# Kernel optimization log

Measured on AMD Instinct MI355X. Metric: run time of the kernel, lower is better.

The kernel has to match this reference:

```python
import jax, jax.numpy as jnp
import numpy as np

N, D, K = 32768, 256, 2048
BETA = 0.25  # init arg beta, in [0,1) branch of the loss


def setup_inputs() -> dict:
    key = jax.random.key(0)
    k1, k2 = jax.random.split(key)
    x = jax.random.normal(k1, (N, D), dtype=jnp.float32)
    # mimics nn.Embedding init: uniform(-1/K, 1/K) then mean-centered
    cb = jax.random.uniform(k2, (K, D), dtype=jnp.float32, minval=-1.0 / K, maxval=1.0 / K)
    codebook = cb - cb.mean(axis=0)
    return {"x": x, "codebook": codebook}


def reference(x, codebook):
    # pairwise squared L2 distances: [N, K]
    dist = (
        jnp.sum(x * x, axis=1, keepdims=True)
        + jnp.sum(codebook * codebook, axis=1)
        - 2.0 * jnp.matmul(x, codebook.T)
    )
    encoding_inds = jnp.argmin(dist, axis=1)  # [N]
    # one-hot @ codebook == gather of nearest code vectors
    x_codebook = jnp.take(codebook, encoding_inds, axis=0)  # [N, D]
    # straight-through quantization
    x_quantized = x + jax.lax.stop_gradient(x_codebook - x)
    # VQ loss, beta in [0, 1) branch
    commit = jnp.mean((x - jax.lax.stop_gradient(x_codebook)) ** 2)
    embed = jnp.mean((x_codebook - jax.lax.stop_gradient(x)) ** 2)
    loss = BETA * commit + embed
    return x_quantized, loss
```

## Files before the change

### kernel.cpp

```cpp
#include <hip/hip_runtime.h>

#define N_ROWS 32768
#define DIM    256
#define KCODES 2048
#define CSCALE 4096.0f

typedef __attribute__((ext_vector_type(16))) float f32x16;
typedef __attribute__((ext_vector_type(4)))  unsigned int u32x4;

union frag16 { u32x4 v; long l[2]; };

#define WAIT_LGKM0 0xC07F
#define WAIT_VM4   0x0F74
#define WAIT_VM0   0x0F70

__device__ __forceinline__ void gl16(const void* g, void* l) {
    __builtin_amdgcn_global_load_lds(
        (const __attribute__((address_space(1))) unsigned int*)g,
        (__attribute__((address_space(3))) unsigned int*)l, 16, 0, 0);
}

__device__ __forceinline__ uint4 pack16(const float* s) {
    int a = __builtin_amdgcn_cvt_pk_fp8_f32(s[0],  s[1],  0, false);
    a     = __builtin_amdgcn_cvt_pk_fp8_f32(s[2],  s[3],  a, true);
    int b = __builtin_amdgcn_cvt_pk_fp8_f32(s[4],  s[5],  0, false);
    b     = __builtin_amdgcn_cvt_pk_fp8_f32(s[6],  s[7],  b, true);
    int c = __builtin_amdgcn_cvt_pk_fp8_f32(s[8],  s[9],  0, false);
    c     = __builtin_amdgcn_cvt_pk_fp8_f32(s[10], s[11], c, true);
    int d = __builtin_amdgcn_cvt_pk_fp8_f32(s[12], s[13], 0, false);
    d     = __builtin_amdgcn_cvt_pk_fp8_f32(s[14], s[15], d, true);
    uint4 o; o.x = a; o.y = b; o.z = c; o.w = d;
    return o;
}


__global__ void prep_cb(const float* __restrict__ cb, unsigned int* __restrict__ cbf8,
                        float* __restrict__ halfcn, float* __restrict__ loss) {
    const int t    = threadIdx.x;
    const int code = blockIdx.x * 4 + (t >> 6);
    const int s    = t & 63;
    if (blockIdx.x == 0 && t == 0) *loss = 0.0f;
    const int kc = s >> 4, d = (s >> 2) & 3, b4 = (s & 3) * 4;
    const int h = d >> 1, q = d & 1;
    const int k0 = kc * 64 + q * 32 + (b4 >> 3) * 16 + h * 8 + (b4 & 7);
    float4 v = *(const float4*)&cb[(size_t)code * DIM + k0];
    int pk = __builtin_amdgcn_cvt_pk_fp8_f32(v.x * CSCALE, v.y * CSCALE, 0, false);
    pk     = __builtin_amdgcn_cvt_pk_fp8_f32(v.z * CSCALE, v.w * CSCALE, pk, true);
    cbf8[(size_t)code * 64 + s] = (unsigned int)pk;
    float ssum = v.x * v.x + v.y * v.y + v.z * v.z + v.w * v.w;
    #pragma unroll
    for (int o = 32; o > 0; o >>= 1) ssum += __shfl_down(ssum, o, 64);
    if (s == 0) halfcn[code] = 0.5f * CSCALE * ssum;
}

__global__ __launch_bounds__(256, 2) void vq_fused(
        const float* __restrict__ x, const float* __restrict__ cb,
        const char* __restrict__ cbf8, const float* __restrict__ halfcn,
        float* __restrict__ out, float* __restrict__ loss) {
    __shared__ char As[4][4096];
    __shared__ char Bs[2][4][4096];
    __shared__ float red[64][4];
    __shared__ int  idxs[64];
    __shared__ float lred[4];

    const int t    = threadIdx.x;
    const int lane = t & 63;
    const int w    = t >> 6;
    const int l32  = lane & 31;
    const int h    = lane >> 5;
    const int row0 = blockIdx.x * 64;

    {
        const int r   = t >> 2;
        const int kc  = t & 3;
        const int key = (r >> 1) & 3;
        const float* src = x + (size_t)(row0 + r) * DIM + kc * 64;
        float buf[16];
        #pragma unroll
        for (int p = 0; p < 4; p++) {
            const int d = p ^ key, hh = d >> 1, qq = d & 1;
            #pragma unroll
            for (int j = 0; j < 4; j++) *(float4*)(buf + j * 4) =
                *(const float4*)(src + qq * 32 + (j >> 1) * 16 + hh * 8 + (j & 1) * 4);
            *(uint4*)(As[kc] + r * 64 + p * 16) = pack16(buf);
        }
    }

    float hcv[8][2];
    #pragma unroll
    for (int p = 0; p < 8; p++) {
        hcv[p][0] = halfcn[p * 256 + w * 64 + l32];
        hcv[p][1] = halfcn[p * 256 + w * 64 + 32 + l32];
    }

    const int lsub = lane >> 2;
    const int lpos = lane & 3;
    auto stageB = [&](int i) {
        const int pass = i >> 2, kc = i & 3;
        char* dst = Bs[i & 1][w];
        #pragma unroll
        for (int r_ = 0; r_ < 4; r_++) {
            const int lc = r_ * 16 + lsub;
            const int g  = lpos ^ ((lc >> 1) & 3);
            const char* src = cbf8 + (size_t)(pass * 256 + w * 64 + lc) * 256
                              + kc * 64 + g * 16;
            gl16(src, dst + r_ * 1024);
        }
    };

    float mp[2][16];
    #pragma unroll
    for (int rt = 0; rt < 2; rt++)
        #pragma unroll
        for (int r = 0; r < 16; r++) mp[rt][r] = -3.0e38f;

    const int key = (l32 >> 1) & 3;
    const int p0  = (h * 2 + 0) ^ key;
    const int p1  = (h * 2 + 1) ^ key;

    __syncthreads();
    stageB(0);

    for (int pass = 0; pass < 8; ++pass) {
        f32x16 acc[2][2];
        #pragma unroll
        for (int rt = 0; rt < 2; rt++)
            #pragma unroll
            for (int r = 0; r < 16; r++) {
                acc[rt][0][r] = -hcv[pass][0];
                acc[rt][1][r] = -hcv[pass][1];
            }

        #pragma unroll
        for (int kc = 0; kc < 4; ++kc) {
            const int i = pass * 4 + kc;
            __builtin_amdgcn_s_waitcnt(WAIT_LGKM0);
            if (i < 31) {
                stageB(i + 1);
                __builtin_amdgcn_s_waitcnt(WAIT_VM4);
            } else {
                __builtin_amdgcn_s_waitcnt(WAIT_VM0);
            }

            const char* ab = As[kc];
            const char* bb = Bs[i & 1][w];
            frag16 af[2][2], bf[2][2];
            #pragma unroll
            for (int rt = 0; rt < 2; rt++) {
                const int rbase = (rt * 32 + l32) * 64;
                af[rt][0].v = *(const u32x4*)(ab + rbase + p0 * 16);
                af[rt][1].v = *(const u32x4*)(ab + rbase + p1 * 16);
            }
            #pragma unroll
            for (int ct = 0; ct < 2; ct++) {
                const int cbase = (ct * 32 + l32) * 64;
                bf[ct][0].v = *(const u32x4*)(bb + cbase + p0 * 16);
                bf[ct][1].v = *(const u32x4*)(bb + cbase + p1 * 16);
            }
            #pragma unroll
            for (int q = 0; q < 2; q++)
                #pragma unroll
                for (int hf = 0; hf < 2; hf++)
                    #pragma unroll
                    for (int rt = 0; rt < 2; rt++)
                        #pragma unroll
                        for (int ct = 0; ct < 2; ct++)
                            acc[rt][ct] = __builtin_amdgcn_mfma_f32_32x32x16_fp8_fp8(
                                af[rt][q].l[hf], bf[ct][q].l[hf], acc[rt][ct], 0, 0, 0);
        }

        #pragma unroll
        for (int ct = 0; ct < 2; ct++) {
            const unsigned code = (unsigned)(pass * 256 + w * 64 + ct * 32 + l32);
            #pragma unroll
            for (int rt = 0; rt < 2; rt++)
                #pragma unroll
                for (int r = 0; r < 16; r++) {
                    unsigned u = (__float_as_uint(acc[rt][ct][r]) & 0xFFFFF800u) | code;
                    mp[rt][r] = fmaxf(mp[rt][r], __uint_as_float(u));
                }
        }
    }

    #pragma unroll
    for (int m = 1; m <= 16; m <<= 1)
        #pragma unroll
        for (int rt = 0; rt < 2; rt++)
            #pragma unroll
            for (int r = 0; r < 16; r++)
                mp[rt][r] = fmaxf(mp[rt][r], __shfl_xor(mp[rt][r], m, 64));

    if (l32 == 0) {
        #pragma unroll
        for (int rt = 0; rt < 2; rt++)
            #pragma unroll
            for (int r = 0; r < 16; r++) {
                const int row = rt * 32 + (r & 3) + 8 * (r >> 2) + 4 * h;
                red[row][w] = mp[rt][r];
            }
    }
    __syncthreads();
    if (t < 64) {
        float b0 = fmaxf(fmaxf(red[t][0], red[t][1]), fmaxf(red[t][2], red[t][3]));
        idxs[t] = (int)(__float_as_uint(b0) & 2047u);
    }
    __syncthreads();

    float lsum = 0.0f;
    #pragma unroll 4
    for (int r = 0; r < 64; r++) {
        const int code = idxs[r];
        const float c  = cb[(size_t)code * DIM + t];
        const float xv = x[(size_t)(row0 + r) * DIM + t];
        out[(size_t)(row0 + r) * DIM + t] = c;
        const float d = xv - c;
        lsum += d * d;
    }
    #pragma unroll
    for (int o = 32; o > 0; o >>= 1) lsum += __shfl_down(lsum, o, 64);
    if (lane == 0) lred[w] = lsum;
    __syncthreads();
    if (t == 0) {
        const float scale = 1.25f / (float)((size_t)N_ROWS * DIM);
        atomicAdd(loss, (lred[0] + lred[1] + lred[2] + lred[3]) * scale);
    }
}

extern "C" void kernel_launch(void* const* d_in, const int* in_sizes, int n_in,
                              void* d_out, int out_size, void* d_ws, size_t ws_size,
                              hipStream_t stream) {
    const float* x  = (const float*)d_in[0];
    const float* cb = (const float*)d_in[1];
    float* out  = (float*)d_out;
    float* loss = out + (size_t)N_ROWS * DIM;

    char* ws = (char*)d_ws;
    unsigned int* cbf8 = (unsigned int*)ws;
    float* halfcn = (float*)(ws + (size_t)KCODES * 256);

    prep_cb<<<KCODES / 4, 256, 0, stream>>>(cb, cbf8, halfcn, loss);
    vq_fused<<<N_ROWS / 64, 256, 0, stream>>>(x, cb, (const char*)cbf8, halfcn, out, loss);
}
```

Baseline: 123.4 us.

## Halve rows per block, keep A fragments in registers, alias shared memory

Each block now handles 32 rows instead of 64. The packed fp8 A tile is loaded once into registers rather than re-read from LDS on every k-chunk. All shared buffers are aliased into one 32 KB region, and launch bounds are raised to 4 blocks per CU, with the halfcn values prefetched one pass ahead. The goal is higher occupancy and less LDS traffic. In exchange the codebook B tile is streamed twice as often per row, since each block still walks all 2048 codes for fewer rows.

```diff
diff --git a/kernel.cpp b/kernel.cpp
--- a/kernel.cpp
+++ b/kernel.cpp
@@ -4,6 +4,7 @@
 #define DIM    256
 #define KCODES 2048
 #define CSCALE 4096.0f
+#define RPB    32
 
 typedef __attribute__((ext_vector_type(16))) float f32x16;
 typedef __attribute__((ext_vector_type(4)))  unsigned int u32x4;
@@ -53,51 +54,55 @@
     if (s == 0) halfcn[code] = 0.5f * CSCALE * ssum;
 }
 
-__global__ __launch_bounds__(256, 2) void vq_fused(
+__global__ __launch_bounds__(256, 4) void vq_fused(
         const float* __restrict__ x, const float* __restrict__ cb,
         const char* __restrict__ cbf8, const float* __restrict__ halfcn,
         float* __restrict__ out, float* __restrict__ loss) {
-    __shared__ char As[4][4096];
-    __shared__ char Bs[2][4][4096];
-    __shared__ float red[64][4];
-    __shared__ int  idxs[64];
-    __shared__ float lred[4];
+    __shared__ char mem[32768];
 
     const int t    = threadIdx.x;
     const int lane = t & 63;
     const int w    = t >> 6;
     const int l32  = lane & 31;
     const int h    = lane >> 5;
-    const int row0 = blockIdx.x * 64;
+    const int row0 = blockIdx.x * RPB;
 
     {
-        const int r   = t >> 2;
-        const int kc  = t & 3;
+        const int r   = t >> 3;
+        const int sub = t & 7;
+        const int kc  = sub >> 1;
+        const int pb  = (sub & 1) * 2;
         const int key = (r >> 1) & 3;
         const float* src = x + (size_t)(row0 + r) * DIM + kc * 64;
         float buf[16];
         #pragma unroll
-        for (int p = 0; p < 4; p++) {
+        for (int pi = 0; pi < 2; pi++) {
+            const int p = pb + pi;
             const int d = p ^ key, hh = d >> 1, qq = d & 1;
             #pragma unroll
             for (int j = 0; j < 4; j++) *(float4*)(buf + j * 4) =
                 *(const float4*)(src + qq * 32 + (j >> 1) * 16 + hh * 8 + (j & 1) * 4);
-            *(uint4*)(As[kc] + r * 64 + p * 16) = pack16(buf);
-        }
-    }
-
-    float hcv[8][2];
-    #pragma unroll
-    for (int p = 0; p < 8; p++) {
-        hcv[p][0] = halfcn[p * 256 + w * 64 + l32];
-        hcv[p][1] = halfcn[p * 256 + w * 64 + 32 + l32];
-    }
+            *(uint4*)(mem + kc * 2048 + r * 64 + p * 16) = pack16(buf);
+        }
+    }
+    __syncthreads();
+
+    const int key = (l32 >> 1) & 3;
+    const int p0  = (h * 2 + 0) ^ key;
+    const int p1  = (h * 2 + 1) ^ key;
+    frag16 afr[4][2];
+    #pragma unroll
+    for (int kc = 0; kc < 4; kc++) {
+        afr[kc][0].v = *(const u32x4*)(mem + kc * 2048 + l32 * 64 + p0 * 16);
+        afr[kc][1].v = *(const u32x4*)(mem + kc * 2048 + l32 * 64 + p1 * 16);
+    }
+    __syncthreads();
 
     const int lsub = lane >> 2;
     const int lpos = lane & 3;
     auto stageB = [&](int i) {
         const int pass = i >> 2, kc = i & 3;
-        char* dst = Bs[i & 1][w];
+        char* dst = mem + (i & 1) * 16384 + w * 4096;
         #pragma unroll
         for (int r_ = 0; r_ < 4; r_++) {
             const int lc = r_ * 16 + lsub;
@@ -108,49 +113,37 @@
         }
     };
 
-    float mp[2][16];
-    #pragma unroll
-    for (int rt = 0; rt < 2; rt++)
-        #pragma unroll
-        for (int r = 0; r < 16; r++) mp[rt][r] = -3.0e38f;
-
-    const int key = (l32 >> 1) & 3;
-    const int p0  = (h * 2 + 0) ^ key;
-    const int p1  = (h * 2 + 1) ^ key;
-
-    __syncthreads();
+    float mp[16];
+    #pragma unroll
+    for (int r = 0; r < 16; r++) mp[r] = -3.0e38f;
+
+    float hc0 = halfcn[w * 64 + l32];
+    float hc1 = halfcn[w * 64 + 32 + l32];
+
     stageB(0);
-
     for (int pass = 0; pass < 8; ++pass) {
-        f32x16 acc[2][2];
-        #pragma unroll
-        for (int rt = 0; rt < 2; rt++)
-            #pragma unroll
-            for (int r = 0; r < 16; r++) {
-                acc[rt][0][r] = -hcv[pass][0];
-                acc[rt][1][r] = -hcv[pass][1];
-            }
+        f32x16 acc[2];
+        #pragma unroll
+        for (int r = 0; r < 16; r++) { acc[0][r] = -hc0; acc[1][r] = -hc1; }
+        float hc0n = 0.0f, hc1n = 0.0f;
+        if (pass < 7) {
+            hc0n = halfcn[(pass + 1) * 256 + w * 64 + l32];
+            hc1n = halfcn[(pass + 1) * 256 + w * 64 + 32 + l32];
+        }
 
         #pragma unroll
         for (int kc = 0; kc < 4; ++kc) {
             const int i = pass * 4 + kc;
             __builtin_amdgcn_s_waitcnt(WAIT_LGKM0);
-            if (i < 31) {
+            if (i + 1 < 32) {
                 stageB(i + 1);
                 __builtin_amdgcn_s_waitcnt(WAIT_VM4);
             } else {
                 __builtin_amdgcn_s_waitcnt(WAIT_VM0);
             }
 
-            const char* ab = As[kc];
-            const char* bb = Bs[i & 1][w];
-            frag16 af[2][2], bf[2][2];
-            #pragma unroll
-            for (int rt = 0; rt < 2; rt++) {
-                const int rbase = (rt * 32 + l32) * 64;
-                af[rt][0].v = *(const u32x4*)(ab + rbase + p0 * 16);
-                af[rt][1].v = *(const u32x4*)(ab + rbase + p1 * 16);
-            }
+            const char* bb = mem + (i & 1) * 16384 + w * 4096;
+            frag16 bf[2][2];
             #pragma unroll
             for (int ct = 0; ct < 2; ct++) {
                 const int cbase = (ct * 32 + l32) * 64;
@@ -162,53 +155,52 @@
                 #pragma unroll
                 for (int hf = 0; hf < 2; hf++)
                     #pragma unroll
-                    for (int rt = 0; rt < 2; rt++)
-                        #pragma unroll
-                        for (int ct = 0; ct < 2; ct++)
-                            acc[rt][ct] = __builtin_amdgcn_mfma_f32_32x32x16_fp8_fp8(
-                                af[rt][q].l[hf], bf[ct][q].l[hf], acc[rt][ct], 0, 0, 0);
+                    for (int ct = 0; ct < 2; ct++)
+                        acc[ct] = __builtin_amdgcn_mfma_f32_32x32x16_fp8_fp8(
+                            afr[kc][q].l[hf], bf[ct][q].l[hf], acc[ct], 0, 0, 0);
         }
 
         #pragma unroll
         for (int ct = 0; ct < 2; ct++) {
             const unsigned code = (unsigned)(pass * 256 + w * 64 + ct * 32 + l32);
             #pragma unroll
-            for (int rt = 0; rt < 2; rt++)
-                #pragma unroll
-                for (int r = 0; r < 16; r++) {
-                    unsigned u = (__float_as_uint(acc[rt][ct][r]) & 0xFFFFF800u) | code;
-                    mp[rt][r] = fmaxf(mp[rt][r], __uint_as_float(u));
-                }
-        }
+            for (int r = 0; r < 16; r++) {
+                unsigned u = (__float_as_uint(acc[ct][r]) & 0xFFFFF800u) | code;
+                mp[r] = fmaxf(mp[r], __uint_as_float(u));
+            }
+        }
+        hc0 = hc0n; hc1 = hc1n;
     }
 
     #pragma unroll
     for (int m = 1; m <= 16; m <<= 1)
         #pragma unroll
-        for (int rt = 0; rt < 2; rt++)
-            #pragma unroll
-            for (int r = 0; r < 16; r++)
-                mp[rt][r] = fmaxf(mp[rt][r], __shfl_xor(mp[rt][r], m, 64));
+        for (int r = 0; r < 16; r++)
+            mp[r] = fmaxf(mp[r], __shfl_xor(mp[r], m, 64));
+
+    __syncthreads();
+    float* red  = (float*)mem;
+    int*   idxs = (int*)(mem + 1024);
+    float* lred = (float*)(mem + 2048);
 
     if (l32 == 0) {
         #pragma unroll
-        for (int rt = 0; rt < 2; rt++)
-            #pragma unroll
-            for (int r = 0; r < 16; r++) {
-                const int row = rt * 32 + (r & 3) + 8 * (r >> 2) + 4 * h;
-                red[row][w] = mp[rt][r];
-            }
-    }
-    __syncthreads();
-    if (t < 64) {
-        float b0 = fmaxf(fmaxf(red[t][0], red[t][1]), fmaxf(red[t][2], red[t][3]));
+        for (int r = 0; r < 16; r++) {
+            const int row = (r & 3) + 8 * (r >> 2) + 4 * h;
+            red[row * 4 + w] = mp[r];
+        }
+    }
+    __syncthreads();
+    if (t < RPB) {
+        float b0 = fmaxf(fmaxf(red[t * 4 + 0], red[t * 4 + 1]),
+                         fmaxf(red[t * 4 + 2], red[t * 4 + 3]));
         idxs[t] = (int)(__float_as_uint(b0) & 2047u);
     }
     __syncthreads();
 
     float lsum = 0.0f;
     #pragma unroll 4
-    for (int r = 0; r < 64; r++) {
+    for (int r = 0; r < RPB; r++) {
         const int code = idxs[r];
         const float c  = cb[(size_t)code * DIM + t];
         const float xv = x[(size_t)(row0 + r) * DIM + t];
@@ -239,5 +231,5 @@
     float* halfcn = (float*)(ws + (size_t)KCODES * 256);
 
     prep_cb<<<KCODES / 4, 256, 0, stream>>>(cb, cbf8, halfcn, loss);
-    vq_fused<<<N_ROWS / 64, 256, 0, stream>>>(x, cb, (const char*)cbf8, halfcn, out, loss);
-}
+    vq_fused<<<N_ROWS / RPB, 256, 0, stream>>>(x, cb, (const char*)cbf8, halfcn, out, loss);
+}
```

Measured after the change: 127.0 us. 1.03x slower.
